# Kernel optimization log

Hardware: AMD Instinct MI355X
Metric: run time of the kernel (lower is better)

Reference implementation:

```python
import jax, jax.numpy as jnp
import numpy as np

N, B, T, H, S = 4096, 64, 128, 128, 3
DT = 0.01
V_MEAN = -75.0
V_STD = 115.0  # 75 + 40


def setup_inputs() -> dict:
    key = jax.random.key(0)
    ks = jax.random.split(key, 17)
    d = {}
    d['v0'] = jax.random.normal(ks[0], (N, B), dtype=jnp.float32)
    d['s0'] = jax.random.uniform(ks[1], (N, B, S), dtype=jnp.float32)
    d['I_s_all'] = jax.random.uniform(ks[2], (T, N, B), dtype=jnp.float32)
    # FEM operators: mass matrix and inverse PDE operator (contractive for stability)
    d['mass'] = jax.random.normal(ks[3], (N, N), dtype=jnp.float32) / N
    d['inv_pde'] = jax.random.normal(ks[4], (N, N), dtype=jnp.float32) / N + 0.9 * jnp.eye(N, dtype=jnp.float32)
    # Forcing MLP: (1+S) -> H -> H -> S
    d['fW1'] = jax.random.normal(ks[5], (1 + S, H), dtype=jnp.float32) / np.sqrt(1 + S)
    d['fb1'] = jnp.zeros((H,), jnp.float32)
    d['fW2'] = jax.random.normal(ks[6], (H, H), dtype=jnp.float32) / np.sqrt(H)
    d['fb2'] = jnp.zeros((H,), jnp.float32)
    d['fW3'] = jax.random.normal(ks[7], (H, S), dtype=jnp.float32) / np.sqrt(H)
    d['fb3'] = jnp.zeros((S,), jnp.float32)
    # Ionic current MLP: (1+S) -> H -> H -> 1
    d['iW1'] = jax.random.normal(ks[8], (1 + S, H), dtype=jnp.float32) / np.sqrt(1 + S)
    d['ib1'] = jnp.zeros((H,), jnp.float32)
    d['iW2'] = jax.random.normal(ks[9], (H, H), dtype=jnp.float32) / np.sqrt(H)
    d['ib2'] = jnp.zeros((H,), jnp.float32)
    d['iW3'] = jax.random.normal(ks[10], (H, 1), dtype=jnp.float32) / np.sqrt(H)
    d['ib3'] = jnp.zeros((1,), jnp.float32)
    return d


def _mlp(x, W1, b1, W2, b2, W3, b3):
    h = jnp.tanh(x @ W1 + b1)
    h = jnp.tanh(h @ W2 + b2)
    return h @ W3 + b3


def reference(v0, s0, I_s_all, mass, inv_pde,
              fW1, fb1, fW2, fb2, fW3, fb3,
              iW1, ib1, iW2, ib2, iW3, ib3):
    def step(carry, I_s):
        v, s = carry  # v: [N,B], s: [N,B,S]
        vn = (v - V_MEAN) / V_STD
        x = jnp.concatenate([vn[..., None], s], axis=-1)  # [N,B,1+S]
        f = _mlp(x, fW1, fb1, fW2, fb2, fW3, fb3)          # forcing -> ds/dt
        s = s + DT * f
        xi = jnp.concatenate([vn[..., None], s], axis=-1)
        I_ion = _mlp(xi, iW1, ib1, iW2, ib2, iW3, ib3)[..., 0] * V_STD + V_MEAN  # [N,B]
        # rhs = M v + dt M I_s - dt M I_ion  (fused into one GEMM)
        rhs = mass @ (v + DT * I_s - DT * I_ion)
        v = inv_pde @ rhs
        return (v, s), None

    (v, s), _ = jax.lax.scan(jax.checkpoint(step), (v0, s0), I_s_all)
    return v
```

## Files before the change

### kernel.cpp

```cpp
#include <hip/hip_runtime.h>
#include <stdint.h>

#define N_     4096
#define B_     64
#define NB_    (N_*B_)
#define T_     128
#define DT_    0.01f
#define VMEAN_ (-75.0f)
#define VSTD_  115.0f

typedef short bf16x8 __attribute__((ext_vector_type(8)));
typedef float f32x4  __attribute__((ext_vector_type(4)));

static __device__ __forceinline__ uint16_t f2bf(float f) {
  union { float f; uint32_t u; } v; v.f = f;
  uint32_t u = v.u;
  return (uint16_t)((u + 0x7FFFu + ((u >> 16) & 1u)) >> 16);
}

static __device__ __forceinline__ float fast_tanh(float x) {
  float ex = __builtin_amdgcn_exp2f(x * 2.8853900817779268f);
  return 1.0f - 2.0f * __builtin_amdgcn_rcpf(ex + 1.0f);
}

static __device__ __forceinline__ f32x4 mfma16(bf16x8 a, bf16x8 b, f32x4 c) {
  return __builtin_amdgcn_mfma_f32_16x16x32_bf16(a, b, c, 0, 0, 0);
}

__global__ void k_prep_small(const float* __restrict__ fW2, const float* __restrict__ iW2,
                             uint16_t* __restrict__ W2fT, uint16_t* __restrict__ W2iT) {
  const float* src = (blockIdx.x == 0) ? fW2 : iW2;
  uint16_t* dst = (blockIdx.x == 0) ? W2fT : W2iT;
  int t = threadIdx.x;
  for (int e = 0; e < 64; ++e) {
    int idx = e * 256 + t;
    int j = idx >> 7, k = idx & 127;
    dst[idx] = f2bf(src[k * 128 + j]);
  }
}

__global__ __launch_bounds__(256) void k_prep_gemm(const float* __restrict__ Ipde,
                                                   const float* __restrict__ Mmat,
                                                   uint16_t* __restrict__ Apre) {
  __shared__ __align__(16) uint16_t Al[128 * 72];
  __shared__ __align__(16) uint16_t Bl[128 * 72];
  int t = threadIdx.x;
  int row0 = (blockIdx.x >> 5) * 128;
  int col0 = (blockIdx.x & 31) * 128;
  int w = t >> 6, l = t & 63;
  int wr = (w >> 1) * 64, wc = (w & 1) * 64;
  f32x4 acc[4][4];
  for (int i = 0; i < 4; ++i)
    for (int j = 0; j < 4; ++j) { f32x4 z = {0.f,0.f,0.f,0.f}; acc[i][j] = z; }
  for (int ch = 0; ch < 64; ++ch) {
    int k0 = ch * 64;
    __syncthreads();
    for (int e = 0; e < 16; ++e) {
      int idx = e * 256 + t;
      int r = idx >> 5;
      int kp = (idx & 31) * 2;
      const float2 f2v = *(const float2*)(Ipde + (size_t)(row0 + r) * 4096 + k0 + kp);
      uint32_t pk = (uint32_t)f2bf(f2v.x) | ((uint32_t)f2bf(f2v.y) << 16);
      *(uint32_t*)&Al[r * 72 + kp] = pk;
    }
    for (int e = 0; e < 32; ++e) {
      int idx = e * 256 + t;
      int kk = idx >> 7, jj = idx & 127;
      Bl[jj * 72 + kk] = f2bf(Mmat[(size_t)(k0 + kk) * 4096 + col0 + jj]);
    }
    __syncthreads();
    for (int ks = 0; ks < 2; ++ks) {
      bf16x8 af[4], bfv[4];
      for (int rt = 0; rt < 4; ++rt)
        af[rt] = *(const bf16x8*)&Al[(wr + rt * 16 + (l & 15)) * 72 + (l >> 4) * 8 + ks * 32];
      for (int ct = 0; ct < 4; ++ct)
        bfv[ct] = *(const bf16x8*)&Bl[(wc + ct * 16 + (l & 15)) * 72 + (l >> 4) * 8 + ks * 32];
      for (int rt = 0; rt < 4; ++rt)
        for (int ct = 0; ct < 4; ++ct)
          acc[rt][ct] = mfma16(af[rt], bfv[ct], acc[rt][ct]);
    }
  }
  for (int rt = 0; rt < 4; ++rt)
    for (int ct = 0; ct < 4; ++ct)
      for (int e = 0; e < 4; ++e) {
        int i = row0 + wr + rt * 16 + (l >> 4) * 4 + e;
        int j = col0 + wc + ct * 16 + (l & 15);
        Apre[(size_t)i * 4096 + j] = f2bf(acc[rt][ct][e]);
      }
}

__global__ __launch_bounds__(256) void k_mlp(
    const float* __restrict__ vsrc, int vparts,
    const float* __restrict__ ssrc, float* __restrict__ sdst,
    const float* __restrict__ Isrc,
    const uint16_t* __restrict__ W2fT, const uint16_t* __restrict__ W2iT,
    const float* __restrict__ fW1, const float* __restrict__ fb1,
    const float* __restrict__ fb2, const float* __restrict__ fW3, const float* __restrict__ fb3,
    const float* __restrict__ iW1, const float* __restrict__ ib1,
    const float* __restrict__ ib2, const float* __restrict__ iW3, const float* __restrict__ ib3,
    uint16_t* __restrict__ uT)
{
  __shared__ __align__(16) uint16_t W2l[128 * 136];
  __shared__ __align__(16) uint16_t hb[64 * 136];
  __shared__ float vls[256];
  __shared__ float sls[256 * 3];
  __shared__ float Ils[256];
  __shared__ float cW1[4 * 128];
  __shared__ float cb1[128];
  __shared__ float cb2[128];
  __shared__ float cW3[128 * 4];
  __shared__ float cb3[4];

  int t = threadIdx.x;
  int p0 = blockIdx.x * 256;
  int w = t >> 6, l = t & 63;

  {
    float v = 0.f;
    for (int ks = 0; ks < vparts; ++ks) v += vsrc[(size_t)ks * NB_ + p0 + t];
    vls[t] = v;
    for (int e = 0; e < 3; ++e) sls[e * 256 + t] = ssrc[(size_t)p0 * 3 + e * 256 + t];
    Ils[t] = Isrc[p0 + t];
  }

  for (int ph = 0; ph < 2; ++ph) {
    const uint16_t* W2g = ph ? W2iT : W2fT;
    const float* W1 = ph ? iW1 : fW1;
    const float* b1 = ph ? ib1 : fb1;
    const float* b2 = ph ? ib2 : fb2;
    const float* W3 = ph ? iW3 : fW3;
    const float* b3 = ph ? ib3 : fb3;
    int n_out = ph ? 1 : 3;
    __syncthreads();
    for (int e = 0; e < 32; ++e) {
      int idx = e * 256 + t;
      int r = idx >> 6, kp = idx & 63;
      ((uint32_t*)&W2l[r * 136])[kp] = ((const uint32_t*)W2g)[r * 64 + kp];
    }
    for (int i = t; i < 512; i += 256) cW1[i] = W1[i];
    if (t < 128) {
      cb1[t] = b1[t];
      cb2[t] = b2[t];
      for (int o = 0; o < n_out; ++o) cW3[t * 4 + o] = W3[t * n_out + o];
    }
    if (t < 4) cb3[t] = (t < n_out) ? b3[t] : 0.f;
    __syncthreads();

    for (int st = 0; st < 4; ++st) {
      int pb = st * 64;
      {
        int pr = t >> 2;
        int part = t & 3;
        int pl = pb + pr;
        float vn = (vls[pl] - VMEAN_) * (1.0f / VSTD_);
        float s0v = sls[pl * 3 + 0], s1v = sls[pl * 3 + 1], s2v = sls[pl * 3 + 2];
        int jbase = part * 32;
        for (int jj = 0; jj < 32; jj += 2) {
          int j = jbase + jj;
          float z0 = cb1[j]     + vn * cW1[j]     + s0v * cW1[128 + j]     + s1v * cW1[256 + j]     + s2v * cW1[384 + j];
          float z1 = cb1[j + 1] + vn * cW1[j + 1] + s0v * cW1[128 + j + 1] + s1v * cW1[256 + j + 1] + s2v * cW1[384 + j + 1];
          uint32_t pk = (uint32_t)f2bf(fast_tanh(z0)) | ((uint32_t)f2bf(fast_tanh(z1)) << 16);
          *(uint32_t*)&hb[pr * 136 + j] = pk;
        }
      }
      __syncthreads();
      f32x4 acc[8];
      for (int ct = 0; ct < 8; ++ct) { f32x4 z = {0.f,0.f,0.f,0.f}; acc[ct] = z; }
      for (int ks = 0; ks < 4; ++ks) {
        bf16x8 a = *(const bf16x8*)&hb[(w * 16 + (l & 15)) * 136 + (l >> 4) * 8 + ks * 32];
        for (int ct = 0; ct < 8; ++ct) {
          bf16x8 b = *(const bf16x8*)&W2l[(ct * 16 + (l & 15)) * 136 + (l >> 4) * 8 + ks * 32];
          acc[ct] = mfma16(a, b, acc[ct]);
        }
      }
      float fa[4][3];
      for (int e = 0; e < 4; ++e) for (int o = 0; o < 3; ++o) fa[e][o] = 0.f;
      for (int ct = 0; ct < 8; ++ct) {
        int j = ct * 16 + (l & 15);
        float bias = cb2[j];
        float w3v[3];
        for (int o = 0; o < n_out; ++o) w3v[o] = cW3[j * 4 + o];
        for (int e = 0; e < 4; ++e) {
          float h2 = fast_tanh(acc[ct][e] + bias);
          for (int o = 0; o < n_out; ++o) fa[e][o] += h2 * w3v[o];
        }
      }
      for (int m = 1; m < 16; m <<= 1)
        for (int e = 0; e < 4; ++e)
          for (int o = 0; o < n_out; ++o)
            fa[e][o] += __shfl_xor(fa[e][o], m, 64);
      if ((l & 15) == 0) {
        for (int e = 0; e < 4; ++e) {
          int pl = pb + w * 16 + (l >> 4) * 4 + e;
          int P = p0 + pl;
          if (ph == 0) {
            for (int o = 0; o < 3; ++o) {
              float snew = sls[pl * 3 + o] + DT_ * (fa[e][o] + cb3[o]);
              sls[pl * 3 + o] = snew;
              sdst[(size_t)P * 3 + o] = snew;
            }
          } else {
            float I_ion = (fa[e][0] + cb3[0]) * VSTD_ + VMEAN_;
            float u = vls[pl] + DT_ * Ils[pl] - DT_ * I_ion;
            int n = P >> 6, b = P & 63;
            uT[(size_t)b * 4096 + n] = f2bf(u);
          }
        }
      }
      __syncthreads();
    }
  }
}

__global__ __launch_bounds__(256) void k_gemm(const uint16_t* __restrict__ Apre,
                                              const uint16_t* __restrict__ uT,
                                              float* __restrict__ partial) {
  __shared__ __align__(16) uint16_t Al[64 * 72];
  __shared__ __align__(16) uint16_t Bl[64 * 72];
  int t = threadIdx.x, w = t >> 6, l = t & 63;
  int ksl = blockIdx.x & 7;
  int i0 = (blockIdx.x >> 3) * 64;
  f32x4 acc[4];
  for (int ct = 0; ct < 4; ++ct) { f32x4 z = {0.f,0.f,0.f,0.f}; acc[ct] = z; }
  for (int ch = 0; ch < 8; ++ch) {
    int k0 = ksl * 512 + ch * 64;
    __syncthreads();
    for (int it = 0; it < 2; ++it) {
      int s = it * 256 + t;
      int r = s >> 3, sl = s & 7;
      uint4 da = *(const uint4*)(Apre + (size_t)(i0 + r) * 4096 + k0 + sl * 8);
      *(uint4*)&Al[r * 72 + sl * 8] = da;
      uint4 db = *(const uint4*)(uT + (size_t)r * 4096 + k0 + sl * 8);
      *(uint4*)&Bl[r * 72 + sl * 8] = db;
    }
    __syncthreads();
    for (int ks = 0; ks < 2; ++ks) {
      bf16x8 a = *(const bf16x8*)&Al[(w * 16 + (l & 15)) * 72 + (l >> 4) * 8 + ks * 32];
      for (int ct = 0; ct < 4; ++ct) {
        bf16x8 b = *(const bf16x8*)&Bl[(ct * 16 + (l & 15)) * 72 + (l >> 4) * 8 + ks * 32];
        acc[ct] = mfma16(a, b, acc[ct]);
      }
    }
  }
  float* dst = partial + (size_t)ksl * NB_;
  for (int ct = 0; ct < 4; ++ct)
    for (int e = 0; e < 4; ++e) {
      int i = i0 + w * 16 + (l >> 4) * 4 + e;
      int b = ct * 16 + (l & 15);
      dst[(size_t)i * 64 + b] = acc[ct][e];
    }
}

__global__ void k_reduce(const float* __restrict__ partial, float* __restrict__ out) {
  int idx = (blockIdx.x * 256 + threadIdx.x) * 4;
  f32x4 s = {0.f, 0.f, 0.f, 0.f};
  for (int ks = 0; ks < 8; ++ks)
    s += *(const f32x4*)(partial + (size_t)ks * NB_ + idx);
  *(f32x4*)(out + idx) = s;
}

extern "C" void kernel_launch(void* const* d_in, const int* in_sizes, int n_in,
                              void* d_out, int out_size, void* d_ws, size_t ws_size,
                              hipStream_t stream) {
  const float* v0   = (const float*)d_in[0];
  const float* s0   = (const float*)d_in[1];
  const float* I_s  = (const float*)d_in[2];
  const float* mass = (const float*)d_in[3];
  const float* ipde = (const float*)d_in[4];
  const float* fW1 = (const float*)d_in[5];
  const float* fb1 = (const float*)d_in[6];
  const float* fW2 = (const float*)d_in[7];
  const float* fb2 = (const float*)d_in[8];
  const float* fW3 = (const float*)d_in[9];
  const float* fb3 = (const float*)d_in[10];
  const float* iW1 = (const float*)d_in[11];
  const float* ib1 = (const float*)d_in[12];
  const float* iW2 = (const float*)d_in[13];
  const float* ib2 = (const float*)d_in[14];
  const float* iW3 = (const float*)d_in[15];
  const float* ib3 = (const float*)d_in[16];

  char* ws = (char*)d_ws;
  uint16_t* Apre   = (uint16_t*)(ws);
  uint16_t* W2fT   = (uint16_t*)(ws + 33554432);
  uint16_t* W2iT   = (uint16_t*)(ws + 33587200);
  float*    sstate = (float*)   (ws + 33619968);
  uint16_t* uT     = (uint16_t*)(ws + 36765696);
  float*    part   = (float*)   (ws + 37289984);

  k_prep_small<<<2, 256, 0, stream>>>(fW2, iW2, W2fT, W2iT);
  k_prep_gemm<<<1024, 256, 0, stream>>>(ipde, mass, Apre);
  for (int t = 0; t < T_; ++t) {
    const float* vsrc = (t == 0) ? v0 : part;
    int vparts = (t == 0) ? 1 : 8;
    const float* ssrc = (t == 0) ? s0 : sstate;
    k_mlp<<<NB_ / 256, 256, 0, stream>>>(vsrc, vparts, ssrc, sstate,
        I_s + (size_t)t * NB_, W2fT, W2iT,
        fW1, fb1, fb2, fW3, fb3, iW1, ib1, ib2, iW3, ib3, uT);
    k_gemm<<<512, 256, 0, stream>>>(Apre, uT, part);
  }
  k_reduce<<<256, 256, 0, stream>>>(part, (float*)d_out);
}
```

Baseline: 25.31 ms.

## Keep MLP weights in registers and prefetch GEMM tiles into registers

The MLP kernel now holds the W2 MFMA fragments, W1, b2 and W3 in registers instead of staging them in shared memory. It processes 128 points per half-block, with layer-1 work spread across hidden units, and packs v and s into one float4 input array. It also sets launch bounds for two blocks per SM. The split-K GEMM kernel loads the next K chunk into registers while MFMAs run on the current LDS tile, overlapping global loads with compute. The cost is much higher register pressure (32 bf16x8 fragments), which may cause spills or lower occupancy.

```diff
diff --git a/kernel.cpp b/kernel.cpp
--- a/kernel.cpp
+++ b/kernel.cpp
@@ -89,7 +89,7 @@
       }
 }
 
-__global__ __launch_bounds__(256) void k_mlp(
+__global__ __launch_bounds__(256, 2) void k_mlp(
     const float* __restrict__ vsrc, int vparts,
     const float* __restrict__ ssrc, float* __restrict__ sdst,
     const float* __restrict__ Isrc,
@@ -100,28 +100,27 @@
     const float* __restrict__ ib2, const float* __restrict__ iW3, const float* __restrict__ ib3,
     uint16_t* __restrict__ uT)
 {
-  __shared__ __align__(16) uint16_t W2l[128 * 136];
-  __shared__ __align__(16) uint16_t hb[64 * 136];
+  __shared__ __align__(16) uint16_t hb[128 * 136];
+  __shared__ __align__(16) float inp[256 * 4];
   __shared__ float vls[256];
-  __shared__ float sls[256 * 3];
   __shared__ float Ils[256];
-  __shared__ float cW1[4 * 128];
-  __shared__ float cb1[128];
-  __shared__ float cb2[128];
-  __shared__ float cW3[128 * 4];
-  __shared__ float cb3[4];
 
   int t = threadIdx.x;
   int p0 = blockIdx.x * 256;
   int w = t >> 6, l = t & 63;
+  int jp = t & 63;
+  int pg = t >> 6;
+  int lq = l >> 4, lr = l & 15;
 
   {
     float v = 0.f;
     for (int ks = 0; ks < vparts; ++ks) v += vsrc[(size_t)ks * NB_ + p0 + t];
     vls[t] = v;
-    for (int e = 0; e < 3; ++e) sls[e * 256 + t] = ssrc[(size_t)p0 * 3 + e * 256 + t];
     Ils[t] = Isrc[p0 + t];
-  }
+    inp[t * 4 + 0] = (v - VMEAN_) * (1.0f / VSTD_);
+    for (int o = 0; o < 3; ++o) inp[t * 4 + 1 + o] = ssrc[(size_t)(p0 + t) * 3 + o];
+  }
+  __syncthreads();
 
   for (int ph = 0; ph < 2; ++ph) {
     const uint16_t* W2g = ph ? W2iT : W2fT;
@@ -131,79 +130,87 @@
     const float* W3 = ph ? iW3 : fW3;
     const float* b3 = ph ? ib3 : fb3;
     int n_out = ph ? 1 : 3;
-    __syncthreads();
-    for (int e = 0; e < 32; ++e) {
-      int idx = e * 256 + t;
-      int r = idx >> 6, kp = idx & 63;
-      ((uint32_t*)&W2l[r * 136])[kp] = ((const uint32_t*)W2g)[r * 64 + kp];
-    }
-    for (int i = t; i < 512; i += 256) cW1[i] = W1[i];
-    if (t < 128) {
-      cb1[t] = b1[t];
-      cb2[t] = b2[t];
-      for (int o = 0; o < n_out; ++o) cW3[t * 4 + o] = W3[t * n_out + o];
-    }
-    if (t < 4) cb3[t] = (t < n_out) ? b3[t] : 0.f;
-    __syncthreads();
-
-    for (int st = 0; st < 4; ++st) {
-      int pb = st * 64;
-      {
-        int pr = t >> 2;
-        int part = t & 3;
-        int pl = pb + pr;
-        float vn = (vls[pl] - VMEAN_) * (1.0f / VSTD_);
-        float s0v = sls[pl * 3 + 0], s1v = sls[pl * 3 + 1], s2v = sls[pl * 3 + 2];
-        int jbase = part * 32;
-        for (int jj = 0; jj < 32; jj += 2) {
-          int j = jbase + jj;
-          float z0 = cb1[j]     + vn * cW1[j]     + s0v * cW1[128 + j]     + s1v * cW1[256 + j]     + s2v * cW1[384 + j];
-          float z1 = cb1[j + 1] + vn * cW1[j + 1] + s0v * cW1[128 + j + 1] + s1v * cW1[256 + j + 1] + s2v * cW1[384 + j + 1];
-          uint32_t pk = (uint32_t)f2bf(fast_tanh(z0)) | ((uint32_t)f2bf(fast_tanh(z1)) << 16);
-          *(uint32_t*)&hb[pr * 136 + j] = pk;
-        }
+
+    float w1r[2][5];
+#pragma unroll
+    for (int h = 0; h < 2; ++h) {
+      int j = jp * 2 + h;
+      w1r[h][0] = b1[j];
+#pragma unroll
+      for (int i = 0; i < 4; ++i) w1r[h][1 + i] = W1[i * 128 + j];
+    }
+    float cb2r[8], w3r[8][3], b3r[3];
+#pragma unroll
+    for (int ct = 0; ct < 8; ++ct) {
+      int j = ct * 16 + lr;
+      cb2r[ct] = b2[j];
+      for (int o = 0; o < 3; ++o) w3r[ct][o] = (o < n_out) ? W3[j * n_out + o] : 0.f;
+    }
+    for (int o = 0; o < 3; ++o) b3r[o] = (o < n_out) ? b3[o] : 0.f;
+
+    bf16x8 bfr[4][8];
+#pragma unroll
+    for (int ks = 0; ks < 4; ++ks)
+#pragma unroll
+      for (int ct = 0; ct < 8; ++ct)
+        bfr[ks][ct] = *(const bf16x8*)&W2g[(ct * 16 + lr) * 128 + lq * 8 + ks * 32];
+
+    for (int hf = 0; hf < 2; ++hf) {
+#pragma unroll 4
+      for (int i = 0; i < 32; ++i) {
+        int row = pg * 32 + i;
+        int pt = hf * 128 + row;
+        f32x4 xi = *(const f32x4*)&inp[pt * 4];
+        float z0 = w1r[0][0] + xi.x * w1r[0][1] + xi.y * w1r[0][2] + xi.z * w1r[0][3] + xi.w * w1r[0][4];
+        float z1 = w1r[1][0] + xi.x * w1r[1][1] + xi.y * w1r[1][2] + xi.z * w1r[1][3] + xi.w * w1r[1][4];
+        uint32_t pk = (uint32_t)f2bf(fast_tanh(z0)) | ((uint32_t)f2bf(fast_tanh(z1)) << 16);
+        ((uint32_t*)hb)[row * 68 + jp] = pk;
       }
       __syncthreads();
-      f32x4 acc[8];
-      for (int ct = 0; ct < 8; ++ct) { f32x4 z = {0.f,0.f,0.f,0.f}; acc[ct] = z; }
-      for (int ks = 0; ks < 4; ++ks) {
-        bf16x8 a = *(const bf16x8*)&hb[(w * 16 + (l & 15)) * 136 + (l >> 4) * 8 + ks * 32];
+#pragma unroll
+      for (int gg = 0; gg < 2; ++gg) {
+        int g = w * 2 + gg;
+        f32x4 acc[8];
+#pragma unroll
+        for (int ct = 0; ct < 8; ++ct) { f32x4 z = {0.f,0.f,0.f,0.f}; acc[ct] = z; }
+#pragma unroll
+        for (int ks = 0; ks < 4; ++ks) {
+          bf16x8 a = *(const bf16x8*)&hb[(g * 16 + lr) * 136 + lq * 8 + ks * 32];
+#pragma unroll
+          for (int ct = 0; ct < 8; ++ct)
+            acc[ct] = mfma16(a, bfr[ks][ct], acc[ct]);
+        }
+        float fa[4][3];
+#pragma unroll
+        for (int e = 0; e < 4; ++e) for (int o = 0; o < 3; ++o) fa[e][o] = 0.f;
+#pragma unroll
         for (int ct = 0; ct < 8; ++ct) {
-          bf16x8 b = *(const bf16x8*)&W2l[(ct * 16 + (l & 15)) * 136 + (l >> 4) * 8 + ks * 32];
-          acc[ct] = mfma16(a, b, acc[ct]);
+#pragma unroll
+          for (int e = 0; e < 4; ++e) {
+            float h2 = fast_tanh(acc[ct][e] + cb2r[ct]);
+            for (int o = 0; o < n_out; ++o) fa[e][o] += h2 * w3r[ct][o];
+          }
         }
-      }
-      float fa[4][3];
-      for (int e = 0; e < 4; ++e) for (int o = 0; o < 3; ++o) fa[e][o] = 0.f;
-      for (int ct = 0; ct < 8; ++ct) {
-        int j = ct * 16 + (l & 15);
-        float bias = cb2[j];
-        float w3v[3];
-        for (int o = 0; o < n_out; ++o) w3v[o] = cW3[j * 4 + o];
-        for (int e = 0; e < 4; ++e) {
-          float h2 = fast_tanh(acc[ct][e] + bias);
-          for (int o = 0; o < n_out; ++o) fa[e][o] += h2 * w3v[o];
-        }
-      }
-      for (int m = 1; m < 16; m <<= 1)
-        for (int e = 0; e < 4; ++e)
-          for (int o = 0; o < n_out; ++o)
-            fa[e][o] += __shfl_xor(fa[e][o], m, 64);
-      if ((l & 15) == 0) {
-        for (int e = 0; e < 4; ++e) {
-          int pl = pb + w * 16 + (l >> 4) * 4 + e;
-          int P = p0 + pl;
-          if (ph == 0) {
-            for (int o = 0; o < 3; ++o) {
-              float snew = sls[pl * 3 + o] + DT_ * (fa[e][o] + cb3[o]);
-              sls[pl * 3 + o] = snew;
-              sdst[(size_t)P * 3 + o] = snew;
+        for (int m = 1; m < 16; m <<= 1)
+          for (int e = 0; e < 4; ++e)
+            for (int o = 0; o < n_out; ++o)
+              fa[e][o] += __shfl_xor(fa[e][o], m, 64);
+        if (lr == 0) {
+#pragma unroll
+          for (int e = 0; e < 4; ++e) {
+            int pl = hf * 128 + g * 16 + lq * 4 + e;
+            int P = p0 + pl;
+            if (ph == 0) {
+              for (int o = 0; o < 3; ++o) {
+                float snew = inp[pl * 4 + 1 + o] + DT_ * (fa[e][o] + b3r[o]);
+                inp[pl * 4 + 1 + o] = snew;
+                sdst[(size_t)P * 3 + o] = snew;
+              }
+            } else {
+              float I_ion = (fa[e][0] + b3r[0]) * VSTD_ + VMEAN_;
+              float u = vls[pl] + DT_ * Ils[pl] - DT_ * I_ion;
+              uT[(size_t)(P & 63) * 4096 + (P >> 6)] = f2bf(u);
             }
-          } else {
-            float I_ion = (fa[e][0] + cb3[0]) * VSTD_ + VMEAN_;
-            float u = vls[pl] + DT_ * Ils[pl] - DT_ * I_ion;
-            int n = P >> 6, b = P & 63;
-            uT[(size_t)b * 4096 + n] = f2bf(u);
           }
         }
       }
@@ -220,26 +227,47 @@
   int t = threadIdx.x, w = t >> 6, l = t & 63;
   int ksl = blockIdx.x & 7;
   int i0 = (blockIdx.x >> 3) * 64;
+  int r0 = t >> 3, sl0 = t & 7;
+  int r1 = 32 + (t >> 3), sl1 = t & 7;
   f32x4 acc[4];
   for (int ct = 0; ct < 4; ++ct) { f32x4 z = {0.f,0.f,0.f,0.f}; acc[ct] = z; }
+
+  uint4 da0, da1, db0, db1;
+  {
+    int k0 = ksl * 512;
+    da0 = *(const uint4*)(Apre + (size_t)(i0 + r0) * 4096 + k0 + sl0 * 8);
+    db0 = *(const uint4*)(uT + (size_t)r0 * 4096 + k0 + sl0 * 8);
+    da1 = *(const uint4*)(Apre + (size_t)(i0 + r1) * 4096 + k0 + sl1 * 8);
+    db1 = *(const uint4*)(uT + (size_t)r1 * 4096 + k0 + sl1 * 8);
+    *(uint4*)&Al[r0 * 72 + sl0 * 8] = da0;
+    *(uint4*)&Bl[r0 * 72 + sl0 * 8] = db0;
+    *(uint4*)&Al[r1 * 72 + sl1 * 8] = da1;
+    *(uint4*)&Bl[r1 * 72 + sl1 * 8] = db1;
+  }
+  __syncthreads();
+
   for (int ch = 0; ch < 8; ++ch) {
-    int k0 = ksl * 512 + ch * 64;
-    __syncthreads();
-    for (int it = 0; it < 2; ++it) {
-      int s = it * 256 + t;
-      int r = s >> 3, sl = s & 7;
-      uint4 da = *(const uint4*)(Apre + (size_t)(i0 + r) * 4096 + k0 + sl * 8);
-      *(uint4*)&Al[r * 72 + sl * 8] = da;
-      uint4 db = *(const uint4*)(uT + (size_t)r * 4096 + k0 + sl * 8);
-      *(uint4*)&Bl[r * 72 + sl * 8] = db;
-    }
-    __syncthreads();
+    if (ch < 7) {
+      int k0 = ksl * 512 + (ch + 1) * 64;
+      da0 = *(const uint4*)(Apre + (size_t)(i0 + r0) * 4096 + k0 + sl0 * 8);
+      db0 = *(const uint4*)(uT + (size_t)r0 * 4096 + k0 + sl0 * 8);
+      da1 = *(const uint4*)(Apre + (size_t)(i0 + r1) * 4096 + k0 + sl1 * 8);
+      db1 = *(const uint4*)(uT + (size_t)r1 * 4096 + k0 + sl1 * 8);
+    }
     for (int ks = 0; ks < 2; ++ks) {
       bf16x8 a = *(const bf16x8*)&Al[(w * 16 + (l & 15)) * 72 + (l >> 4) * 8 + ks * 32];
       for (int ct = 0; ct < 4; ++ct) {
         bf16x8 b = *(const bf16x8*)&Bl[(ct * 16 + (l & 15)) * 72 + (l >> 4) * 8 + ks * 32];
         acc[ct] = mfma16(a, b, acc[ct]);
       }
+    }
+    __syncthreads();
+    if (ch < 7) {
+      *(uint4*)&Al[r0 * 72 + sl0 * 8] = da0;
+      *(uint4*)&Bl[r0 * 72 + sl0 * 8] = db0;
+      *(uint4*)&Al[r1 * 72 + sl1 * 8] = da1;
+      *(uint4*)&Bl[r1 * 72 + sl1 * 8] = db1;
+      __syncthreads();
     }
   }
   float* dst = partial + (size_t)ksl * NB_;
```

Result: faster. 21.74 ms (-14.1%).
